# Optimization experiments

Hardware: AMD Instinct MI355X
Metric: run time of the kernel (lower is better)

The kernel has to match this reference:

```python
import jax, jax.numpy as jnp
import numpy as np

B, N, E, H, R, L, VOCAB, KINDS = 8, 4096, 524288, 128, 8, 2, 100000, 8


def setup_inputs() -> dict:
    key = jax.random.key(0)
    ks = jax.random.split(key, 12)
    concept_ids = jax.random.randint(ks[0], (B, N), 1, VOCAB)  # avoid padding_idx 0
    kind_ids = jax.random.randint(ks[1], (B, N), 0, KINDS)
    node_mask = jnp.ones((B, N), dtype=jnp.int32)
    # edges constrained within each batch block (module assumes per-subgraph edges)
    e_batch = jax.random.randint(ks[2], (E,), 0, B)
    src = e_batch * N + jax.random.randint(ks[3], (E,), 0, N)
    dst = e_batch * N + jax.random.randint(ks[4], (E,), 0, N)
    edge_index = jnp.stack([src, dst], axis=0)
    edge_type = jax.random.randint(ks[5], (E,), 0, R)
    s = 0.02
    concept_emb = jax.random.normal(ks[6], (VOCAB, H), jnp.float32) * s
    concept_emb = concept_emb.at[0].set(0.0)  # padding_idx=0
    kind_emb = jax.random.normal(ks[7], (KINDS, H), jnp.float32) * s
    proj_W = jax.random.normal(ks[8], (H, H), jnp.float32) * s
    proj_b = jnp.zeros((H,), jnp.float32)
    self_W = jax.random.normal(ks[9], (L, H, H), jnp.float32) * s
    self_b = jnp.zeros((L, H), jnp.float32)
    rel_W = jax.random.normal(ks[10], (L, R, H, H), jnp.float32) * s
    return dict(pkg_node_concept_ids=concept_ids, pkg_node_kind_ids=kind_ids,
                pkg_node_mask=node_mask, pkg_edge_index=edge_index,
                pkg_edge_type=edge_type, concept_emb=concept_emb, kind_emb=kind_emb,
                proj_W=proj_W, proj_b=proj_b, self_W=self_W, self_b=self_b, rel_W=rel_W)


def reference(pkg_node_concept_ids, pkg_node_kind_ids, pkg_node_mask,
              pkg_edge_index, pkg_edge_type, concept_emb, kind_emb,
              proj_W, proj_b, self_W, self_b, rel_W):
    b, n = pkg_node_concept_ids.shape
    num_nodes = b * n
    # input embedding + projection (dropout = identity in eval)
    x = concept_emb[pkg_node_concept_ids] + kind_emb[pkg_node_kind_ids]  # [B,N,H]
    x = jnp.einsum('bnh,gh->bng', x, proj_W) + proj_b
    x = x.reshape(num_nodes, -1)  # packed node states [B*N, H]
    src, dst = pkg_edge_index[0], pkg_edge_index[1]
    deg = jax.ops.segment_sum(jnp.ones_like(src, dtype=x.dtype), dst,
                              num_segments=num_nodes)[:, None]
    deg = jnp.maximum(deg, 1.0)
    n_layers, n_rel = rel_W.shape[0], rel_W.shape[1]
    for l in range(n_layers):
        xs = x[src]  # [E,H] gather
        msgs = jnp.zeros_like(xs)
        for r in range(n_rel):
            msgs = msgs + jnp.where((pkg_edge_type == r)[:, None],
                                    xs @ rel_W[l, r].T, 0.0)
        agg = jax.ops.segment_sum(msgs, dst, num_segments=num_nodes) / deg
        x = jax.nn.relu(x @ self_W[l].T + self_b[l] + agg)
    out = x.reshape(b, n, -1) * pkg_node_mask[..., None].astype(x.dtype)
    return out
```

## Files before the change

kernel.cpp:

```cpp
#include <hip/hip_runtime.h>
#include <hip/hip_bf16.h>

#define NODES 32768
#define HD 128
#define NE 524288
#define NR 8
#define NS 262144
#define PASSB 65536

typedef unsigned int u32;
typedef unsigned short u16;
typedef __attribute__((ext_vector_type(8))) short bf16x8;
typedef __attribute__((ext_vector_type(4))) float f32x4;

#define XH_OFF   (0u)
#define XL_OFF   (8u<<20)
#define XH2_OFF  (16u<<20)
#define XL2_OFF  (24u<<20)
#define ADJ_OFF  (32u<<20)
#define RP_OFF   (34u<<20)
#define CUR_OFF  (36u<<20)
#define BSUM_OFF (37u<<20)
#define BP_OFF   (38u<<20)

#define BP_LAYER 294912
#define PP_ELEM  589824

__device__ __forceinline__ float bflo(u32 u){ union{u32 i;float f;}c; c.i=u<<16; return c.f; }
__device__ __forceinline__ float bfhi(u32 u){ union{u32 i;float f;}c; c.i=u&0xffff0000u; return c.f; }
__device__ __forceinline__ u16 f2bf(float f){
  u32 u=__float_as_uint(f);
  u32 r=u + 0x7fffu + ((u>>16)&1u);
  return (u16)(r>>16);
}
__device__ __forceinline__ float bf2f(u16 h){ return __uint_as_float(((u32)h)<<16); }

__device__ __forceinline__ void gl_lds16(const void* g, void* l){
  __builtin_amdgcn_global_load_lds((const __attribute__((address_space(1))) u32*)g,
                                   (__attribute__((address_space(3))) u32*)l, 16, 0, 0);
}

__global__ void prep_w(const float* __restrict__ rW, const float* __restrict__ sW,
                       const float* __restrict__ pWg, u16* __restrict__ Bp)
{
  int idx=blockIdx.x*256+threadIdx.x;
  if(idx<294912){
    int l=idx/147456;
    int rem=idx%147456;
    int t=rem>>14;
    int kn=rem&16383;
    int k=kn>>7, n=kn&127;
    float w;
    if(t<8) w=rW[(((size_t)l*NR+t)*HD+n)*HD+k];
    else    w=sW[((size_t)l*HD+n)*HD+k];
    u16* base=Bp+(size_t)l*BP_LAYER+(size_t)t*32768;
    int ks=k>>5, q=(k>>3)&3, j=k&7;
    size_t off=((size_t)ks*128+n)*32+q*8+j;
    u16 hb=f2bf(w);
    u16 lb=f2bf(w-bf2f(hb));
    base[off]=hb;
    base[off+16384]=lb;
  } else {
    int kn=idx-294912;
    int k=kn>>7, n=kn&127;
    float w=pWg[(size_t)n*HD+k];
    u16* base=Bp+PP_ELEM;
    int ks=k>>5, q=(k>>3)&3, j=k&7;
    size_t off=((size_t)ks*128+n)*32+q*8+j;
    u16 hb=f2bf(w);
    u16 lb=f2bf(w-bf2f(hb));
    base[off]=hb;
    base[off+16384]=lb;
  }
}

__global__ __launch_bounds__(256,2) void embed_mfma(
    const int* __restrict__ cid, const int* __restrict__ kid,
    const float* __restrict__ cemb, const float* __restrict__ kemb,
    const u16* __restrict__ PP, const float* __restrict__ pb,
    u16* __restrict__ xh, u16* __restrict__ xl)
{
  __shared__ u16 Atile[2][128*128];
  const int tid=threadIdx.x;
  const int wave=tid>>6, lane=tid&63;
  const int wm=wave>>1, wn=wave&1;
  const int q=lane>>4;
  const int d0=blockIdx.x*128;

  { int r=tid>>1, half=tid&1;
    int ci=cid[d0+r], ki=kid[d0+r];
    const float* cp=cemb+(size_t)ci*HD+half*64;
    const float* kp=kemb+(size_t)ki*HD+half*64;
#pragma unroll
    for(int cc=0;cc<8;cc++){
      float4 a0=*(const float4*)(cp+cc*8);
      float4 a1=*(const float4*)(cp+cc*8+4);
      float4 b0=*(const float4*)(kp+cc*8);
      float4 b1=*(const float4*)(kp+cc*8+4);
      float v[8]={a0.x+b0.x,a0.y+b0.y,a0.z+b0.z,a0.w+b0.w,
                  a1.x+b1.x,a1.y+b1.y,a1.z+b1.z,a1.w+b1.w};
      u16 hb[8], lb[8];
#pragma unroll
      for(int j=0;j<8;j++){ hb[j]=f2bf(v[j]); lb[j]=f2bf(v[j]-bf2f(hb[j])); }
      int chunk=half*8+cc;
      int dst=r*128+(chunk^(r&15))*8;
      uint4 hv={(u32)hb[0]|((u32)hb[1]<<16),(u32)hb[2]|((u32)hb[3]<<16),
                (u32)hb[4]|((u32)hb[5]<<16),(u32)hb[6]|((u32)hb[7]<<16)};
      uint4 lv={(u32)lb[0]|((u32)lb[1]<<16),(u32)lb[2]|((u32)lb[3]<<16),
                (u32)lb[4]|((u32)lb[5]<<16),(u32)lb[6]|((u32)lb[7]<<16)};
      *(uint4*)&Atile[0][dst]=hv;
      *(uint4*)&Atile[1][dst]=lv;
    }
  }
  __syncthreads();

  f32x4 acc[4][4];
#pragma unroll
  for(int a=0;a<4;a++)
#pragma unroll
    for(int b=0;b<4;b++) acc[a][b]=(f32x4){0.f,0.f,0.f,0.f};

#pragma unroll
  for(int ks=0;ks<4;ks++){
    bf16x8 ah[4];
#pragma unroll
    for(int tm=0;tm<4;tm++){
      int m=wm*64+tm*16+(lane&15);
      ah[tm]=*(const bf16x8*)&Atile[0][m*128+(((ks*4)+q)^(m&15))*8];
    }
#pragma unroll
    for(int s=0;s<2;s++){
      const u16* Bb=PP+s*16384;
#pragma unroll
      for(int tn=0;tn<4;tn++){
        int n=wn*64+tn*16+(lane&15);
        bf16x8 bfr=*(const bf16x8*)&Bb[((size_t)ks*128+n)*32+q*8];
#pragma unroll
        for(int tm=0;tm<4;tm++)
          acc[tm][tn]=__builtin_amdgcn_mfma_f32_16x16x32_bf16(ah[tm],bfr,acc[tm][tn],0,0,0);
      }
    }
  }
#pragma unroll
  for(int ks=0;ks<4;ks++){
    bf16x8 al[4];
#pragma unroll
    for(int tm=0;tm<4;tm++){
      int m=wm*64+tm*16+(lane&15);
      al[tm]=*(const bf16x8*)&Atile[1][m*128+(((ks*4)+q)^(m&15))*8];
    }
#pragma unroll
    for(int tn=0;tn<4;tn++){
      int n=wn*64+tn*16+(lane&15);
      bf16x8 bfr=*(const bf16x8*)&PP[((size_t)ks*128+n)*32+q*8];
#pragma unroll
      for(int tm=0;tm<4;tm++)
        acc[tm][tn]=__builtin_amdgcn_mfma_f32_16x16x32_bf16(al[tm],bfr,acc[tm][tn],0,0,0);
    }
  }

  __syncthreads();
  { u16* Sh=(u16*)Atile[0];
    u16* Sl=(u16*)Atile[1];
#pragma unroll
    for(int tn=0;tn<4;tn++){
      int n=wn*64+tn*16+(lane&15);
      float b=pb[n];
#pragma unroll
      for(int tm=0;tm<4;tm++){
        int rbase=wm*64+tm*16+q*4;
#pragma unroll
        for(int r=0;r<4;r++){
          float v=acc[tm][tn][r]+b;
          u16 hb=f2bf(v);
          u16 lb=f2bf(v-bf2f(hb));
          int row=rbase+r;
          u32 ab=(u32)(row*256+n*2);
          ab^=((u32)((row>>2)&3))<<5;
          Sh[ab>>1]=hb;
          Sl[ab>>1]=lb;
        }
      }
    }
  }
  __syncthreads();
  { const char* S0=(const char*)Atile[0];
    const char* S1=(const char*)Atile[1];
    char* xhb=(char*)(xh+(size_t)d0*HD);
    char* xlb=(char*)(xl+(size_t)d0*HD);
#pragma unroll
    for(int i=0;i<8;i++){
      u32 byte=(u32)(i*256+tid)*16;
      u32 row=byte>>8;
      u32 lb2=byte^((((row>>2)&3))<<5);
      *(uint4*)(xhb+byte)=*(const uint4*)(S0+lb2);
      *(uint4*)(xlb+byte)=*(const uint4*)(S1+lb2);
    }
  }
}

__global__ void count_deg2(const int* __restrict__ dst, const int* __restrict__ et,
                           u32* __restrict__ cnt){
  int e=blockIdx.x*256+threadIdx.x;
  int t=et[e];
  int d=dst[e];
  int key=(d>>5)*256 + t*32 + (d&31);
  atomicAdd(&cnt[key],1u);
}

__global__ void scan1(u32* __restrict__ cnt, u32* __restrict__ rp, u32* __restrict__ bsum){
  __shared__ u32 sh[256];
  int t=threadIdx.x; int base=blockIdx.x*256;
  u32 v=cnt[base+t]; sh[t]=v;
  cnt[base+t]=0u;
  __syncthreads();
  for(int off=1;off<256;off<<=1){
    u32 tv=(t>=off)?sh[t-off]:0u; __syncthreads();
    sh[t]+=tv; __syncthreads();
  }
  rp[base+t]=sh[t]-v;
  if(t==255) bsum[blockIdx.x]=sh[255];
}

__global__ void scan2b(u32* __restrict__ bsum, u32* __restrict__ rp){
  __shared__ u32 sh[256];
  int t=threadIdx.x;
  u32 v0=bsum[t*4+0],v1=bsum[t*4+1],v2=bsum[t*4+2],v3=bsum[t*4+3];
  u32 s=v0+v1+v2+v3;
  sh[t]=s; __syncthreads();
  for(int off=1;off<256;off<<=1){
    u32 tv=(t>=off)?sh[t-off]:0u; __syncthreads();
    sh[t]+=tv; __syncthreads();
  }
  u32 ex=sh[t]-s;
  bsum[t*4+0]=ex; bsum[t*4+1]=ex+v0; bsum[t*4+2]=ex+v0+v1; bsum[t*4+3]=ex+v0+v1+v2;
  if(t==0) rp[NS]=NE;
  if(t==255) bsum[1024]=0u;
}

__global__ void scatter_edges2(const int* __restrict__ src, const int* __restrict__ dst,
                               const int* __restrict__ et, const u32* __restrict__ rp,
                               const u32* __restrict__ bsum,
                               u32* __restrict__ cur, u32* __restrict__ adj){
  int e=blockIdx.x*256+threadIdx.x;
  int t=et[e];
  int d=dst[e];
  int key=(d>>5)*256 + t*32 + (d&31);
  u32 pos=atomicAdd(&cur[key],1u);
  u32 row=(u32)((t<<5)|(d&31));
  adj[rp[key]+bsum[key>>8]+pos]=(u32)src[e] | (row<<15);
}

__global__ __launch_bounds__(256,2) void fused_layer(
    const u16* __restrict__ xh, const u16* __restrict__ xl,
    const u16* __restrict__ Bp,
    const u32* __restrict__ rp, const u32* __restrict__ bsum,
    const u32* __restrict__ adj,
    const float* __restrict__ sb, const int* __restrict__ mask,
    u16* __restrict__ oh, u16* __restrict__ ol, float* __restrict__ outf, int last)
{
  __shared__ u16 As16[256*128];
  __shared__ float sdeg[32];
  const int tid=threadIdx.x;
  const int wave=tid>>6, lane=tid&63;
  const int q=lane>>4;
  const int d0=blockIdx.x*32;
  const u32* xh32=(const u32*)xh;

  { uint4 zz={0u,0u,0u,0u};
    uint4* p4=(uint4*)As16;
#pragma unroll
    for(int i=0;i<16;i++) p4[wave*1024 + i*64 + lane]=zz;
  }

#define FLUSH1(rw) do{ \
    u32 u0=__float_as_uint(v0), u1=__float_as_uint(v1); \
    u32 hp=(u1&0xffff0000u)|(u0>>16); \
    int fw=(rw)*64 + (((lane>>2)^((rw)&15))<<2) + (lane&3); \
    ((u32*)As16)[fw]=hp; \
  }while(0)
  { u32 kb=(u32)(blockIdx.x*256 + wave*64);
    u32 beg=rp[kb]+bsum[kb>>8];
    u32 ke=kb+64u;
    u32 end=rp[ke]+bsum[ke>>8];
    int currow=-1; float v0=0.f,v1=0.f;
    for(u32 base=beg; base<end; base+=64u){
      int nk=(int)(end-base); if(nk>64) nk=64;
      u32 adjv=(lane<nk)?adj[base+lane]:0u;
      u32 hA[32], hB[32];
#pragma unroll
      for(int j=0;j<32;j++)
        hA[j]=xh32[(size_t)((u32)__builtin_amdgcn_readlane((int)adjv,j)&0x7fffu)*64+lane];
#pragma unroll
      for(int j=0;j<32;j++)
        hB[j]=xh32[(size_t)((u32)__builtin_amdgcn_readlane((int)adjv,j+32)&0x7fffu)*64+lane];
#pragma unroll
      for(int j=0;j<32;j++){
        if(j<nk){
          u32 w=(u32)__builtin_amdgcn_readlane((int)adjv,j);
          int r=(int)(w>>15);
          if(r!=currow){ if(currow>=0) FLUSH1(currow); currow=r; v0=0.f; v1=0.f; }
          v0+=bflo(hA[j]); v1+=bfhi(hA[j]);
        }
      }
#pragma unroll
      for(int j=0;j<32;j++){
        if(j+32<nk){
          u32 w=(u32)__builtin_amdgcn_readlane((int)adjv,j+32);
          int r=(int)(w>>15);
          if(r!=currow){ if(currow>=0) FLUSH1(currow); currow=r; v0=0.f; v1=0.f; }
          v0+=bflo(hB[j]); v1+=bfhi(hB[j]);
        }
      }
    }
    if(currow>=0) FLUSH1(currow);
  }
#undef FLUSH1
  __syncthreads();

  f32x4 accR[2][2];
#pragma unroll
  for(int a=0;a<2;a++)
#pragma unroll
    for(int b=0;b<2;b++) accR[a][b]=(f32x4){0.f,0.f,0.f,0.f};
#pragma unroll
  for(int rl=0;rl<8;rl++){
    const u16* Bt=Bp+(size_t)rl*32768;
#pragma unroll
    for(int ks=0;ks<4;ks++){
      bf16x8 ah[2];
#pragma unroll
      for(int mf=0;mf<2;mf++){
        int ar=rl*32+mf*16+(lane&15);
        ah[mf]=*(const bf16x8*)&As16[ar*128+((((ks<<2)+q)^(ar&15))<<3)];
      }
#pragma unroll
      for(int tn=0;tn<2;tn++){
        int n=wave*32+tn*16+(lane&15);
        bf16x8 bh=*(const bf16x8*)&Bt[((size_t)(ks*128+n))*32+q*8];
#pragma unroll
        for(int mf=0;mf<2;mf++)
          accR[mf][tn]=__builtin_amdgcn_mfma_f32_16x16x32_bf16(ah[mf],bh,accR[mf][tn],0,0,0);
      }
    }
  }
  __syncthreads();

#pragma unroll
  for(int i=0;i<2;i++){
    int rbase=wave*8+i*4;
    int r=rbase+(lane>>4);
    int g=(lane&15)^(r&15);
    gl_lds16(xh+(size_t)(d0+r)*HD+g*8, &As16[rbase*128]);
    gl_lds16(xl+(size_t)(d0+r)*HD+g*8, &As16[(32+rbase)*128]);
  }
  if(tid<32){
    int g=d0+tid; u32 dg=0;
#pragma unroll
    for(int et=0;et<8;et++){
      u32 k=(u32)(blockIdx.x*256 + et*32 + tid);
      dg+=(rp[k+1]+bsum[(k+1)>>8])-(rp[k]+bsum[k>>8]);
    }
    sdeg[tid]=1.f/fmaxf((float)dg,1.f);
  }
  __syncthreads();

  f32x4 accS[2][2];
#pragma unroll
  for(int a=0;a<2;a++)
#pragma unroll
    for(int b=0;b<2;b++) accS[a][b]=(f32x4){0.f,0.f,0.f,0.f};
  { const u16* Bt=Bp+(size_t)8*32768;
#pragma unroll
    for(int ks=0;ks<4;ks++){
      bf16x8 ah[2],al[2];
#pragma unroll
      for(int mf=0;mf<2;mf++){
        int ar=mf*16+(lane&15);
        int sw=((((ks<<2)+q)^(ar&15))<<3);
        ah[mf]=*(const bf16x8*)&As16[ar*128+sw];
        al[mf]=*(const bf16x8*)&As16[(32+ar)*128+sw];
      }
#pragma unroll
      for(int tn=0;tn<2;tn++){
        int n=wave*32+tn*16+(lane&15);
        size_t boff=((size_t)(ks*128+n))*32+q*8;
        bf16x8 bh=*(const bf16x8*)&Bt[boff];
        bf16x8 bl=*(const bf16x8*)&Bt[boff+16384];
#pragma unroll
        for(int mf=0;mf<2;mf++){
          accS[mf][tn]=__builtin_amdgcn_mfma_f32_16x16x32_bf16(ah[mf],bh,accS[mf][tn],0,0,0);
          accS[mf][tn]=__builtin_amdgcn_mfma_f32_16x16x32_bf16(al[mf],bh,accS[mf][tn],0,0,0);
          accS[mf][tn]=__builtin_amdgcn_mfma_f32_16x16x32_bf16(ah[mf],bl,accS[mf][tn],0,0,0);
        }
      }
    }
  }

#pragma unroll
  for(int tn=0;tn<2;tn++){
    int n=wave*32+tn*16+(lane&15);
    float bb=sb[n];
    if(last){
#pragma unroll
      for(int mf=0;mf<2;mf++)
#pragma unroll
        for(int rr=0;rr<4;rr++){
          int row=mf*16+q*4+rr;
          float v=fmaxf(accS[mf][tn][rr]+bb+accR[mf][tn][rr]*sdeg[row],0.f);
          v*=(float)mask[d0+row];
          outf[(size_t)(d0+row)*HD+n]=v;
        }
    } else {
#pragma unroll
      for(int mf=0;mf<2;mf++)
#pragma unroll
        for(int rr=0;rr<4;rr++){
          int row=mf*16+q*4+rr;
          float v=fmaxf(accS[mf][tn][rr]+bb+accR[mf][tn][rr]*sdeg[row],0.f);
          u16 hb=f2bf(v);
          u16 lb=f2bf(v-bf2f(hb));
          oh[(size_t)(d0+row)*HD+n]=hb;
          ol[(size_t)(d0+row)*HD+n]=lb;
        }
    }
  }
}

extern "C" void kernel_launch(void* const* d_in, const int* in_sizes, int n_in,
                              void* d_out, int out_size, void* d_ws, size_t ws_size,
                              hipStream_t stream)
{
  (void)in_sizes; (void)n_in; (void)out_size; (void)ws_size;
  const int*   cid =(const int*)  d_in[0];
  const int*   kid =(const int*)  d_in[1];
  const int*   mask=(const int*)  d_in[2];
  const int*   ei  =(const int*)  d_in[3];
  const int*   et  =(const int*)  d_in[4];
  const float* cemb=(const float*)d_in[5];
  const float* kemb=(const float*)d_in[6];
  const float* pW  =(const float*)d_in[7];
  const float* pb  =(const float*)d_in[8];
  const float* sW  =(const float*)d_in[9];
  const float* sb  =(const float*)d_in[10];
  const float* rW  =(const float*)d_in[11];
  float* out=(float*)d_out;
  char*  ws =(char*)d_ws;

  u16* xh =(u16*)(ws+XH_OFF);
  u16* xl =(u16*)(ws+XL_OFF);
  u16* xh2=(u16*)(ws+XH2_OFF);
  u16* xl2=(u16*)(ws+XL2_OFF);
  u32* adj =(u32*)(ws+ADJ_OFF);
  u32* rp  =(u32*)(ws+RP_OFF);
  u32* cur =(u32*)(ws+CUR_OFF);
  u32* bsum=(u32*)(ws+BSUM_OFF);
  u16* Bp  =(u16*)(ws+BP_OFF);
  const int* srcA=ei;
  const int* dstA=ei+NE;

  hipMemsetAsync(cur,0,NS*sizeof(u32),stream);
  prep_w<<<1216,256,0,stream>>>(rW,sW,pW,Bp);
  embed_mfma<<<NODES/128,256,0,stream>>>(cid,kid,cemb,kemb,Bp+PP_ELEM,pb,xh,xl);
  count_deg2<<<NE/256,256,0,stream>>>(dstA,et,cur);
  scan1<<<NS/256,256,0,stream>>>(cur,rp,bsum);
  scan2b<<<1,256,0,stream>>>(bsum,rp);
  scatter_edges2<<<NE/256,256,0,stream>>>(srcA,dstA,et,rp,bsum,cur,adj);

  fused_layer<<<NODES/32,256,0,stream>>>(xh,xl,Bp,rp,bsum,adj,sb,mask,xh2,xl2,out,0);
  fused_layer<<<NODES/32,256,0,stream>>>(xh2,xl2,Bp+BP_LAYER,rp,bsum,adj,sb+HD,mask,xh,xl,out,1);
}
```

Before: 307.4 us.

## Process relations in phases with 64-node blocks and branchless register aggregation

Reorders the CSR key to relation-major (type*NODES + dst) so each relation forms a contiguous segment. The fused layer now processes one relation at a time: it aggregates into an LDS tile for 64 destination nodes, then runs that relation's MFMA, using 512-thread blocks arranged as a 2x4 wave grid. This shrinks LDS from 64KB to 32KB and replaces the branchy per-row flush with indicator FMAs into eight per-wave row accumulators. The cost is eight barrier-separated phases per block and many redundant FMAs per gathered edge.

```diff
diff --git a/kernel.cpp b/kernel.cpp
--- a/kernel.cpp
+++ b/kernel.cpp
@@ -6,7 +6,6 @@
 #define NE 524288
 #define NR 8
 #define NS 262144
-#define PASSB 65536
 
 typedef unsigned int u32;
 typedef unsigned short u16;
@@ -202,9 +201,7 @@
 __global__ void count_deg2(const int* __restrict__ dst, const int* __restrict__ et,
                            u32* __restrict__ cnt){
   int e=blockIdx.x*256+threadIdx.x;
-  int t=et[e];
-  int d=dst[e];
-  int key=(d>>5)*256 + t*32 + (d&31);
+  int key=et[e]*NODES + dst[e];
   atomicAdd(&cnt[key],1u);
 }
 
@@ -243,15 +240,13 @@
                                const u32* __restrict__ bsum,
                                u32* __restrict__ cur, u32* __restrict__ adj){
   int e=blockIdx.x*256+threadIdx.x;
-  int t=et[e];
   int d=dst[e];
-  int key=(d>>5)*256 + t*32 + (d&31);
+  int key=et[e]*NODES + d;
   u32 pos=atomicAdd(&cur[key],1u);
-  u32 row=(u32)((t<<5)|(d&31));
-  adj[rp[key]+bsum[key>>8]+pos]=(u32)src[e] | (row<<15);
-}
-
-__global__ __launch_bounds__(256,2) void fused_layer(
+  adj[rp[key]+bsum[key>>8]+pos]=(u32)src[e] | (((u32)(d&63))<<15);
+}
+
+__global__ __launch_bounds__(512,2) void fused_layer(
     const u16* __restrict__ xh, const u16* __restrict__ xl,
     const u16* __restrict__ Bp,
     const u32* __restrict__ rp, const u32* __restrict__ bsum,
@@ -259,106 +254,99 @@
     const float* __restrict__ sb, const int* __restrict__ mask,
     u16* __restrict__ oh, u16* __restrict__ ol, float* __restrict__ outf, int last)
 {
-  __shared__ u16 As16[256*128];
-  __shared__ float sdeg[32];
+  __shared__ u32 As32w[8192];
+  __shared__ float sdeg[64];
+  u16* As16=(u16*)As32w;
   const int tid=threadIdx.x;
   const int wave=tid>>6, lane=tid&63;
+  const int wm=wave>>2, wn=wave&3;
   const int q=lane>>4;
-  const int d0=blockIdx.x*32;
+  const int d0=blockIdx.x*64;
   const u32* xh32=(const u32*)xh;
 
-  { uint4 zz={0u,0u,0u,0u};
-    uint4* p4=(uint4*)As16;
-#pragma unroll
-    for(int i=0;i<16;i++) p4[wave*1024 + i*64 + lane]=zz;
-  }
-
-#define FLUSH1(rw) do{ \
-    u32 u0=__float_as_uint(v0), u1=__float_as_uint(v1); \
-    u32 hp=(u1&0xffff0000u)|(u0>>16); \
-    int fw=(rw)*64 + (((lane>>2)^((rw)&15))<<2) + (lane&3); \
-    ((u32*)As16)[fw]=hp; \
-  }while(0)
-  { u32 kb=(u32)(blockIdx.x*256 + wave*64);
-    u32 beg=rp[kb]+bsum[kb>>8];
-    u32 ke=kb+64u;
-    u32 end=rp[ke]+bsum[ke>>8];
-    int currow=-1; float v0=0.f,v1=0.f;
-    for(u32 base=beg; base<end; base+=64u){
-      int nk=(int)(end-base); if(nk>64) nk=64;
-      u32 adjv=(lane<nk)?adj[base+lane]:0u;
-      u32 hA[32], hB[32];
-#pragma unroll
-      for(int j=0;j<32;j++)
-        hA[j]=xh32[(size_t)((u32)__builtin_amdgcn_readlane((int)adjv,j)&0x7fffu)*64+lane];
-#pragma unroll
-      for(int j=0;j<32;j++)
-        hB[j]=xh32[(size_t)((u32)__builtin_amdgcn_readlane((int)adjv,j+32)&0x7fffu)*64+lane];
-#pragma unroll
-      for(int j=0;j<32;j++){
-        if(j<nk){
+  f32x4 accR[2][2];
+#pragma unroll
+  for(int a=0;a<2;a++)
+#pragma unroll
+    for(int b=0;b<2;b++) accR[a][b]=(f32x4){0.f,0.f,0.f,0.f};
+
+  for(int p=0;p<8;p++){
+    float v0[8], v1[8];
+#pragma unroll
+    for(int r=0;r<8;r++){ v0[r]=0.f; v1[r]=0.f; }
+    { u32 kb=(u32)(p*NODES + d0 + wave*8);
+      u32 beg=rp[kb]+bsum[kb>>8];
+      u32 ke=kb+8u;
+      u32 end=rp[ke]+bsum[ke>>8];
+      for(u32 base=beg; base<end; base+=32u){
+        int nk=(int)(end-base); if(nk>32) nk=32;
+        u32 adjv=(lane<nk)?adj[base+lane]:0u;
+        u32 h[32];
+#pragma unroll
+        for(int j=0;j<32;j++){
           u32 w=(u32)__builtin_amdgcn_readlane((int)adjv,j);
-          int r=(int)(w>>15);
-          if(r!=currow){ if(currow>=0) FLUSH1(currow); currow=r; v0=0.f; v1=0.f; }
-          v0+=bflo(hA[j]); v1+=bfhi(hA[j]);
-        }
-      }
-#pragma unroll
-      for(int j=0;j<32;j++){
-        if(j+32<nk){
-          u32 w=(u32)__builtin_amdgcn_readlane((int)adjv,j+32);
-          int r=(int)(w>>15);
-          if(r!=currow){ if(currow>=0) FLUSH1(currow); currow=r; v0=0.f; v1=0.f; }
-          v0+=bflo(hB[j]); v1+=bfhi(hB[j]);
-        }
-      }
-    }
-    if(currow>=0) FLUSH1(currow);
-  }
-#undef FLUSH1
-  __syncthreads();
-
-  f32x4 accR[2][2];
-#pragma unroll
-  for(int a=0;a<2;a++)
-#pragma unroll
-    for(int b=0;b<2;b++) accR[a][b]=(f32x4){0.f,0.f,0.f,0.f};
-#pragma unroll
-  for(int rl=0;rl<8;rl++){
-    const u16* Bt=Bp+(size_t)rl*32768;
-#pragma unroll
-    for(int ks=0;ks<4;ks++){
-      bf16x8 ah[2];
-#pragma unroll
-      for(int mf=0;mf<2;mf++){
-        int ar=rl*32+mf*16+(lane&15);
-        ah[mf]=*(const bf16x8*)&As16[ar*128+((((ks<<2)+q)^(ar&15))<<3)];
-      }
-#pragma unroll
-      for(int tn=0;tn<2;tn++){
-        int n=wave*32+tn*16+(lane&15);
-        bf16x8 bh=*(const bf16x8*)&Bt[((size_t)(ks*128+n))*32+q*8];
-#pragma unroll
-        for(int mf=0;mf<2;mf++)
-          accR[mf][tn]=__builtin_amdgcn_mfma_f32_16x16x32_bf16(ah[mf],bh,accR[mf][tn],0,0,0);
-      }
-    }
-  }
-  __syncthreads();
+          h[j]=xh32[(size_t)(w&0x7fffu)*64+lane];
+        }
+#pragma unroll
+        for(int j=0;j<32;j++){
+          u32 w=(u32)__builtin_amdgcn_readlane((int)adjv,j);
+          int row=(int)(w>>15);
+          u32 sm=(j<nk)?0xffffffffu:0u;
+          u32 hm=h[j]&sm;
+          float fl=bflo(hm), fh=bfhi(hm);
+#pragma unroll
+          for(int r=0;r<8;r++){
+            float ind=(row==(wave*8+r))?1.0f:0.0f;
+            v0[r]=__builtin_fmaf(ind,fl,v0[r]);
+            v1[r]=__builtin_fmaf(ind,fh,v1[r]);
+          }
+        }
+      }
+    }
+#pragma unroll
+    for(int r=0;r<8;r++){
+      int row=wave*8+r;
+      u32 u0=__float_as_uint(v0[r]), u1=__float_as_uint(v1[r]);
+      u32 hp=(u1&0xffff0000u)|(u0>>16);
+      int fw=row*64+(((lane>>2)^(row&15))<<2)+(lane&3);
+      As32w[fw]=hp;
+    }
+    __syncthreads();
+    { const u16* Bt=Bp+(size_t)p*32768;
+#pragma unroll
+      for(int ks=0;ks<4;ks++){
+        bf16x8 ah[2];
+#pragma unroll
+        for(int mf=0;mf<2;mf++){
+          int ar=wm*32+mf*16+(lane&15);
+          ah[mf]=*(const bf16x8*)&As16[ar*128+((((ks<<2)+q)^(ar&15))<<3)];
+        }
+#pragma unroll
+        for(int tn=0;tn<2;tn++){
+          int n=wn*32+tn*16+(lane&15);
+          bf16x8 bh=*(const bf16x8*)&Bt[((size_t)(ks*128+n))*32+q*8];
+#pragma unroll
+          for(int mf=0;mf<2;mf++)
+            accR[mf][tn]=__builtin_amdgcn_mfma_f32_16x16x32_bf16(ah[mf],bh,accR[mf][tn],0,0,0);
+        }
+      }
+    }
+    __syncthreads();
+  }
 
 #pragma unroll
   for(int i=0;i<2;i++){
     int rbase=wave*8+i*4;
     int r=rbase+(lane>>4);
     int g=(lane&15)^(r&15);
-    gl_lds16(xh+(size_t)(d0+r)*HD+g*8, &As16[rbase*128]);
-    gl_lds16(xl+(size_t)(d0+r)*HD+g*8, &As16[(32+rbase)*128]);
-  }
-  if(tid<32){
+    gl_lds16(xh+(size_t)(d0+r)*HD+g*8, (char*)As32w + rbase*256);
+    gl_lds16(xl+(size_t)(d0+r)*HD+g*8, (char*)As32w + 16384 + rbase*256);
+  }
+  if(tid<64){
     int g=d0+tid; u32 dg=0;
 #pragma unroll
-    for(int et=0;et<8;et++){
-      u32 k=(u32)(blockIdx.x*256 + et*32 + tid);
+    for(int ph=0;ph<8;ph++){
+      u32 k=(u32)(ph*NODES+g);
       dg+=(rp[k+1]+bsum[(k+1)>>8])-(rp[k]+bsum[k>>8]);
     }
     sdeg[tid]=1.f/fmaxf((float)dg,1.f);
@@ -376,14 +364,14 @@
       bf16x8 ah[2],al[2];
 #pragma unroll
       for(int mf=0;mf<2;mf++){
-        int ar=mf*16+(lane&15);
-        int sw=((((ks<<2)+q)^(ar&15))<<3);
-        ah[mf]=*(const bf16x8*)&As16[ar*128+sw];
-        al[mf]=*(const bf16x8*)&As16[(32+ar)*128+sw];
+        int ar=wm*32+mf*16+(lane&15);
+        int off=ar*128+((((ks<<2)+q)^(ar&15))<<3);
+        ah[mf]=*(const bf16x8*)&As16[off];
+        al[mf]=*(const bf16x8*)&As16[8192+off];
       }
 #pragma unroll
       for(int tn=0;tn<2;tn++){
-        int n=wave*32+tn*16+(lane&15);
+        int n=wn*32+tn*16+(lane&15);
         size_t boff=((size_t)(ks*128+n))*32+q*8;
         bf16x8 bh=*(const bf16x8*)&Bt[boff];
         bf16x8 bl=*(const bf16x8*)&Bt[boff+16384];
@@ -399,14 +387,14 @@
 
 #pragma unroll
   for(int tn=0;tn<2;tn++){
-    int n=wave*32+tn*16+(lane&15);
+    int n=wn*32+tn*16+(lane&15);
     float bb=sb[n];
     if(last){
 #pragma unroll
       for(int mf=0;mf<2;mf++)
 #pragma unroll
         for(int rr=0;rr<4;rr++){
-          int row=mf*16+q*4+rr;
+          int row=wm*32+mf*16+q*4+rr;
           float v=fmaxf(accS[mf][tn][rr]+bb+accR[mf][tn][rr]*sdeg[row],0.f);
           v*=(float)mask[d0+row];
           outf[(size_t)(d0+row)*HD+n]=v;
@@ -416,7 +404,7 @@
       for(int mf=0;mf<2;mf++)
 #pragma unroll
         for(int rr=0;rr<4;rr++){
-          int row=mf*16+q*4+rr;
+          int row=wm*32+mf*16+q*4+rr;
           float v=fmaxf(accS[mf][tn][rr]+bb+accR[mf][tn][rr]*sdeg[row],0.f);
           u16 hb=f2bf(v);
           u16 lb=f2bf(v-bf2f(hb));
@@ -467,6 +455,6 @@
   scan2b<<<1,256,0,stream>>>(bsum,rp);
   scatter_edges2<<<NE/256,256,0,stream>>>(srcA,dstA,et,rp,bsum,cur,adj);
 
-  fused_layer<<<NODES/32,256,0,stream>>>(xh,xl,Bp,rp,bsum,adj,sb,mask,xh2,xl2,out,0);
-  fused_layer<<<NODES/32,256,0,stream>>>(xh2,xl2,Bp+BP_LAYER,rp,bsum,adj,sb+HD,mask,xh,xl,out,1);
-}
+  fused_layer<<<NODES/64,512,0,stream>>>(xh,xl,Bp,rp,bsum,adj,sb,mask,xh2,xl2,out,0);
+  fused_layer<<<NODES/64,512,0,stream>>>(xh2,xl2,Bp+BP_LAYER,rp,bsum,adj,sb+HD,mask,xh,xl,out,1);
+}
```

New measurement: 403.4 us. 31.2% more time.
